# Kernel optimization log

Hardware: AMD Instinct MI355X
Metric: run time of the kernel (lower is better)

## Reference

```python
import jax, jax.numpy as jnp
import numpy as np

N = 20000
E = 320000
H = 16
C = 16
NUM_GRAPHS = 64
NEG_SLOPE = 0.2


def _gat(x, edge_index, W, a_src, a_dst, bias):
    # PyG GATConv, concat=True, shared lin for src/dst, eval mode (no dropout)
    h = (x @ W).reshape(-1, H, C)                       # [N,H,C]
    src, dst = edge_index[0], edge_index[1]
    alpha_src = jnp.sum(h * a_src, axis=-1)             # [N,H]
    alpha_dst = jnp.sum(h * a_dst, axis=-1)             # [N,H]
    alpha = alpha_src[src] + alpha_dst[dst]             # [E,H]
    alpha = jax.nn.leaky_relu(alpha, NEG_SLOPE)
    amax = jax.ops.segment_max(alpha, dst, num_segments=N)
    ex = jnp.exp(alpha - amax[dst])
    denom = jax.ops.segment_sum(ex, dst, num_segments=N)
    attn = ex / jnp.where(denom == 0, 1.0, denom)[dst]  # [E,H]
    msg = h[src] * attn[:, :, None]                     # [E,H,C]
    out = jax.ops.segment_sum(msg, dst, num_segments=N) # [N,H,C]
    return out.reshape(-1, H * C) + bias


def setup_inputs() -> dict:
    key = jax.random.key(0)
    ks = jax.random.split(key, 32)
    d = {}
    d['x'] = jax.random.normal(ks[0], (N, 20), dtype=jnp.float32)
    d['edge_index_ipv6'] = jax.random.randint(ks[1], (2, E), 0, N)
    d['edge_attr_ipv6'] = jax.random.normal(ks[2], (E, 19), dtype=jnp.float32)
    d['edge_index_tsch'] = jax.random.randint(ks[3], (2, E), 0, N)
    d['edge_attr_tsch'] = jax.random.normal(ks[4], (E, 7), dtype=jnp.float32)
    d['batch'] = jnp.sort(jax.random.randint(ks[5], (N,), 0, NUM_GRAPHS))
    s = 0.1
    d['W_i'] = jax.random.normal(ks[6], (20, H * C), dtype=jnp.float32) * s
    d['a_src_i'] = jax.random.normal(ks[7], (H, C), dtype=jnp.float32) * s
    d['a_dst_i'] = jax.random.normal(ks[8], (H, C), dtype=jnp.float32) * s
    d['b_i'] = jnp.zeros((H * C,), dtype=jnp.float32)
    d['W_t'] = jax.random.normal(ks[9], (20, H * C), dtype=jnp.float32) * s
    d['a_src_t'] = jax.random.normal(ks[10], (H, C), dtype=jnp.float32) * s
    d['a_dst_t'] = jax.random.normal(ks[11], (H, C), dtype=jnp.float32) * s
    d['b_t'] = jnp.zeros((H * C,), dtype=jnp.float32)
    d['Wf'] = jax.random.normal(ks[12], (512, 64), dtype=jnp.float32) * s
    d['bf'] = jnp.zeros((64,), dtype=jnp.float32)
    d['W1'] = jax.random.normal(ks[13], (64, 32), dtype=jnp.float32) * s
    d['b1'] = jnp.zeros((32,), dtype=jnp.float32)
    d['W2'] = jax.random.normal(ks[14], (32, 16), dtype=jnp.float32) * s
    d['b2'] = jnp.zeros((16,), dtype=jnp.float32)
    d['W3'] = jax.random.normal(ks[15], (16, 16), dtype=jnp.float32) * s
    d['b3'] = jnp.zeros((16,), dtype=jnp.float32)
    d['Wce'] = jax.random.normal(ks[16], (16, 3), dtype=jnp.float32) * s
    d['bce'] = jnp.zeros((3,), dtype=jnp.float32)
    d['Wcv'] = jax.random.normal(ks[17], (16, 3), dtype=jnp.float32) * s
    d['bcv'] = jnp.zeros((3,), dtype=jnp.float32)
    return d


def reference(x, edge_index_ipv6, edge_attr_ipv6, edge_index_tsch, edge_attr_tsch,
              batch, W_i, a_src_i, a_dst_i, b_i, W_t, a_src_t, a_dst_t, b_t,
              Wf, bf, W1, b1, W2, b2, W3, b3, Wce, bce, Wcv, bcv):
    # edge_attr_* are ignored by GATConv (edge_dim=None in PyG), as in original
    n_ipv6 = _gat(x, edge_index_ipv6, W_i, a_src_i, a_dst_i, b_i)
    n_tsch = _gat(x, edge_index_tsch, W_t, a_src_t, a_dst_t, b_t)
    h = jnp.concatenate([n_ipv6, n_tsch], axis=-1)      # [N,512]
    h = jax.nn.relu(h @ Wf + bf)
    h = jax.nn.relu(h @ W1 + b1)
    h = jax.nn.relu(h @ W2 + b2)
    h = jax.nn.relu(h @ W3 + b3)                        # [N,16]
    ssum = jax.ops.segment_sum(h, batch, num_segments=NUM_GRAPHS)
    cnt = jax.ops.segment_sum(jnp.ones((h.shape[0], 1), h.dtype), batch,
                              num_segments=NUM_GRAPHS)
    g = ssum / jnp.where(cnt == 0, 1.0, cnt)            # [G,16]
    out_event = g @ Wce + bce
    out_env = g @ Wcv + bcv
    return out_event, out_env
```

## Files before the change

kernel.cpp:

```cpp
#include <hip/hip_runtime.h>
#include <math.h>

#define N_NODES 20000
#define N_EDGES 320000
#define NG 64
#define NEG 0.2f
#define NCHUNK ((N_NODES + 255) / 256)

typedef __attribute__((ext_vector_type(8))) short bf16x8;
typedef __attribute__((ext_vector_type(4))) float f32x4;

__device__ __forceinline__ unsigned short f2bf(float f) {
  unsigned int u = __float_as_uint(f);
  return (unsigned short)((u + 0x7fffu + ((u >> 16) & 1u)) >> 16);
}

__global__ __launch_bounds__(256) void k_prep(
    const float* __restrict__ W_i, const float* __restrict__ as_i, const float* __restrict__ ad_i,
    const float* __restrict__ W_t, const float* __restrict__ as_t, const float* __restrict__ ad_t,
    const float* __restrict__ Wf, const float* __restrict__ bf,
    const float* __restrict__ b_i, const float* __restrict__ b_t,
    float* __restrict__ wsall, unsigned short* __restrict__ wbigfrag,
    float* __restrict__ bfold,
    int* __restrict__ fill_i, int* __restrict__ fill_t,
    float* __restrict__ gsum, int* __restrict__ gcnt) {
  __shared__ float bred[4][64];
  int idx = blockIdx.x * 256 + threadIdx.x;
  if (idx < 1280) {
    int k = idx >> 6, c = idx & 63;
    int set = c >> 5, role = (c >> 4) & 1, h = c & 15;
    const float* W = set ? W_t : W_i;
    const float* a = set ? (role ? ad_t : as_t) : (role ? ad_i : as_i);
    float v = 0.f;
#pragma unroll
    for (int j = 0; j < 16; ++j) v = fmaf(W[k * 256 + h * 16 + j], a[h * 16 + j], v);
    wsall[idx] = v;
    return;
  }
  idx -= 1280;
  if (idx < 49152) {
    int ct = idx / 12288, rem = idx % 12288;
    int lane = (rem >> 3) & 63, j = rem & 7, ks = rem >> 9;
    int k = ks * 32 + ((lane >> 4) << 3) + j;
    int nc = ct * 16 + (lane & 15);
    float v = 0.f;
    int g = (k >= 384) ? 1 : 0;
    int r = k - g * 384;
    int h = r / 24, c = r - h * 24;
    if (c < 20) {
      const float* W = g ? W_t : W_i;
      const float* wr = W + c * 256 + (h << 4);
      const float* wf = Wf + ((g << 8) + (h << 4)) * 64 + nc;
#pragma unroll
      for (int m = 0; m < 16; ++m) v = fmaf(wr[m], wf[m * 64], v);
    }
    wbigfrag[idx] = f2bf(v);
    return;
  }
  idx -= 49152;
  if (idx < 256) {
    int t = threadIdx.x, wv = t >> 6, j = t & 63;
    float p = 0.f;
    int i0 = wv * 128;
#pragma unroll 4
    for (int i = i0; i < i0 + 128; ++i) {
      float b = (i < 256) ? b_i[i] : b_t[i - 256];
      p = fmaf(b, Wf[i * 64 + j], p);
    }
    bred[wv][j] = p;
    __syncthreads();
    if (wv == 0) bfold[j] = bred[0][j] + bred[1][j] + bred[2][j] + bred[3][j] + bf[j];
    return;
  }
  idx -= 256;
  if (idx < N_NODES) { fill_i[idx] = 0; return; }
  idx -= N_NODES;
  if (idx < N_NODES) { fill_t[idx] = 0; return; }
  idx -= N_NODES;
  if (idx < NG * 16) { gsum[idx] = 0.f; return; }
  idx -= NG * 16;
  if (idx < NG) gcnt[idx] = 0;
}

__global__ __launch_bounds__(256) void k_alpha(
    const float* __restrict__ x, const float* __restrict__ wsall,
    float* __restrict__ xpad,
    float* __restrict__ asrc0, float* __restrict__ adst0,
    float* __restrict__ asrc1, float* __restrict__ adst1) {
  int t = threadIdx.x;
  int n0 = blockIdx.x * 16;
  __shared__ float xs[16][20];
  __shared__ float ws[20][64];
  for (int i = t; i < 16 * 20; i += 256) {
    int nd = i / 20, k = i % 20;
    xs[nd][k] = x[(n0 + nd) * 20 + k];
  }
  for (int i = t; i < 1280; i += 256) ws[i >> 6][i & 63] = wsall[i];
  __syncthreads();
  for (int i = t; i < 512; i += 256) {
    int nd = i >> 5, j = i & 31;
    xpad[(size_t)(n0 + nd) * 32 + j] = (j < 20) ? xs[nd][j] : 0.f;
  }
#pragma unroll
  for (int i = 0; i < 4; ++i) {
    int wi = i * 256 + t;
    int nd = wi >> 6, c = wi & 63;
    float v = 0.f;
#pragma unroll
    for (int k = 0; k < 20; ++k) v = fmaf(xs[nd][k], ws[k][c], v);
    int n = n0 + nd, h = c & 15;
    float* arr = (c >> 5) ? ((c >> 4) & 1 ? adst1 : asrc1)
                          : ((c >> 4) & 1 ? adst0 : asrc0);
    arr[n * 16 + h] = v;
  }
}

__global__ void k_hist(const int* __restrict__ ei0, const int* __restrict__ ei1,
                       int* __restrict__ cnt0, int* __restrict__ cnt1) {
  int e = blockIdx.x * blockDim.x + threadIdx.x;
  if (e >= N_EDGES) return;
  if (blockIdx.y == 0)
    atomicAdd(&cnt0[ei0[N_EDGES + e]], 1);
  else
    atomicAdd(&cnt1[ei1[N_EDGES + e]], 1);
}

__global__ __launch_bounds__(256) void k_scan1(
    const int* __restrict__ cnt0, const int* __restrict__ cnt1,
    int* __restrict__ tmp0, int* __restrict__ tmp1, int* __restrict__ csums) {
  int chunk = blockIdx.x, set = blockIdx.y;
  const int* cnt = set ? cnt1 : cnt0;
  int* tmp = set ? tmp1 : tmp0;
  int t = threadIdx.x, lane = t & 63, wv = t >> 6;
  int i = chunk * 256 + t;
  int v = (i < N_NODES) ? cnt[i] : 0;
  int s = v;
#pragma unroll
  for (int d = 1; d < 64; d <<= 1) {
    int o = __shfl_up(s, d);
    if (lane >= d) s += o;
  }
  __shared__ int wsum[4];
  if (lane == 63) wsum[wv] = s;
  __syncthreads();
  int pre = 0;
#pragma unroll
  for (int j = 0; j < 4; ++j)
    if (j < wv) pre += wsum[j];
  s += pre;
  if (i < N_NODES) tmp[i] = s;
  if (t == 255) csums[set * 128 + chunk] = s;
}

__global__ __launch_bounds__(256) void k_scan3(
    const int* __restrict__ tmp0, const int* __restrict__ tmp1,
    const int* __restrict__ csums,
    int* __restrict__ rp0, int* __restrict__ rp1,
    int* __restrict__ fill0, int* __restrict__ fill1) {
  int chunk = blockIdx.x, set = blockIdx.y;
  const int* tmp = set ? tmp1 : tmp0;
  int* rp = set ? rp1 : rp0;
  int* fill = set ? fill1 : fill0;
  __shared__ int soff;
  if (threadIdx.x == 0) {
    int acc = 0;
    for (int cc = 0; cc < chunk; ++cc) acc += csums[set * 128 + cc];
    soff = acc;
  }
  __syncthreads();
  int off = soff;
  int i = chunk * 256 + threadIdx.x;
  if (i >= N_NODES) return;
  int incl = tmp[i];
  int c = fill[i];
  int excl = off + incl - c;
  rp[i] = excl;
  fill[i] = excl;
  if (i == N_NODES - 1) rp[N_NODES] = off + incl;
}

__global__ void k_scatter(const int* __restrict__ ei0, const int* __restrict__ ei1,
                          int* __restrict__ fill0, int* __restrict__ fill1,
                          unsigned short* __restrict__ srcs0,
                          unsigned short* __restrict__ srcs1) {
  int e = blockIdx.x * blockDim.x + threadIdx.x;
  if (e >= N_EDGES) return;
  const int* ei = blockIdx.y ? ei1 : ei0;
  int* fill = blockIdx.y ? fill1 : fill0;
  unsigned short* srcs = blockIdx.y ? srcs1 : srcs0;
  int d = ei[N_EDGES + e];
  int pos = atomicAdd(&fill[d], 1);
  srcs[pos] = (unsigned short)ei[e];
}

__global__ __launch_bounds__(256) void k_gat(
    const float* __restrict__ xpad,
    const float* __restrict__ asrc0, const float* __restrict__ adst0,
    const float* __restrict__ asrc1, const float* __restrict__ adst1,
    const int* __restrict__ rp0, const unsigned short* __restrict__ srcs0,
    const int* __restrict__ rp1, const unsigned short* __restrict__ srcs1,
    unsigned short* __restrict__ xagg) {
  __shared__ float lds[4][416];
  int w4 = threadIdx.x >> 6, lane = threadIdx.x & 63;
  int n = blockIdx.x * 2 + (w4 >> 1);
  int g = w4 & 1;
  int h16 = lane & 15, e4 = lane >> 4;
  float* lxs = lds[w4];
  float* lat = lds[w4] + 288;

  const float* asrc = g ? asrc1 : asrc0;
  const float* adst = g ? adst1 : adst0;
  const int* rp = g ? rp1 : rp0;
  const unsigned short* srcs = g ? srcs1 : srcs0;
  int k0 = rp[n], k1 = rp[n + 1];
  int deg = k1 - k0;
  float adn = adst[n * 16 + h16];
  float lacc = 0.f;
  float xa[8];
#pragma unroll
  for (int j = 0; j < 8; ++j) xa[j] = 0.f;

  if (deg > 0) {
    int nbat = (deg + 7) >> 3;
    int s0a = (int)srcs[min(k0 + e4, k1 - 1)];
    int s0b = (int)srcs[min(k0 + 4 + e4, k1 - 1)];
    float av0a = asrc[s0a * 16 + h16];
    float av0b = asrc[s0b * 16 + h16];
    float2 xv0a = *(const float2*)&xpad[(size_t)s0a * 32 + h16 * 2];
    float2 xv0b = *(const float2*)&xpad[(size_t)s0b * 32 + h16 * 2];
    int s1a = 0, s1b = 0;
    if (nbat > 1) {
      s1a = (int)srcs[min(k0 + 8 + e4, k1 - 1)];
      s1b = (int)srcs[min(k0 + 12 + e4, k1 - 1)];
    }
    for (int bb = 0; bb < nbat; ++bb) {
      float av1a = 0.f, av1b = 0.f;
      float2 xv1a = {0.f, 0.f}, xv1b = {0.f, 0.f};
      int s2a = 0, s2b = 0;
      if (bb + 1 < nbat) {
        av1a = asrc[s1a * 16 + h16];
        av1b = asrc[s1b * 16 + h16];
        xv1a = *(const float2*)&xpad[(size_t)s1a * 32 + h16 * 2];
        xv1b = *(const float2*)&xpad[(size_t)s1b * 32 + h16 * 2];
      }
      if (bb + 2 < nbat) {
        int kb = k0 + (bb + 2) * 8;
        s2a = (int)srcs[min(kb + e4, k1 - 1)];
        s2b = (int)srcs[min(kb + 4 + e4, k1 - 1)];
      }
      int base = k0 + bb * 8;
      float a1 = av0a + adn; a1 = a1 >= 0.f ? a1 : NEG * a1;
      float a2 = av0b + adn; a2 = a2 >= 0.f ? a2 : NEG * a2;
      float exa = (base + e4 < k1) ? __expf(a1) : 0.f;
      float exb = (base + 4 + e4 < k1) ? __expf(a2) : 0.f;
      lacc += exa + exb;
      lat[e4 * 16 + h16] = exa;
      lat[(4 + e4) * 16 + h16] = exb;
      *(float2*)&lxs[e4 * 36 + h16 * 2] = xv0a;
      *(float2*)&lxs[(4 + e4) * 36 + h16 * 2] = xv0b;
#pragma unroll
      for (int e = 0; e < 8; ++e) {
        float w = lat[e * 16 + h16];
        const float4 x0 = *(const float4*)&lxs[e * 36 + e4 * 8];
        const float4 x1 = *(const float4*)&lxs[e * 36 + e4 * 8 + 4];
        xa[0] = fmaf(w, x0.x, xa[0]); xa[1] = fmaf(w, x0.y, xa[1]);
        xa[2] = fmaf(w, x0.z, xa[2]); xa[3] = fmaf(w, x0.w, xa[3]);
        xa[4] = fmaf(w, x1.x, xa[4]); xa[5] = fmaf(w, x1.y, xa[5]);
        xa[6] = fmaf(w, x1.z, xa[6]); xa[7] = fmaf(w, x1.w, xa[7]);
      }
      av0a = av1a; av0b = av1b; xv0a = xv1a; xv0b = xv1b;
      s0a = s1a; s0b = s1b; s1a = s2a; s1b = s2b;
    }
  }
  float lh = lacc + __shfl_xor(lacc, 16);
  lh += __shfl_xor(lh, 32);
  float invl = lh > 0.f ? 1.f / lh : 0.f;
  if (e4 < 3) {
    unsigned int u[4];
#pragma unroll
    for (int q = 0; q < 4; ++q)
      u[q] = (unsigned int)f2bf(xa[2 * q] * invl) |
             ((unsigned int)f2bf(xa[2 * q + 1] * invl) << 16);
    *(uint4*)&xagg[(size_t)n * 768 + g * 384 + h16 * 24 + e4 * 8] = *(uint4*)u;
  }
}

__global__ __launch_bounds__(256) void k_mlp(
    const unsigned short* __restrict__ xagg, const unsigned short* __restrict__ wbigfrag,
    const float* __restrict__ bfold,
    const float* __restrict__ W1m, const float* __restrict__ b1v,
    const float* __restrict__ W2m, const float* __restrict__ b2v,
    const float* __restrict__ W3m, const float* __restrict__ b3v,
    const int* __restrict__ batch,
    float* __restrict__ gsum, int* __restrict__ gcnt) {
  int t = threadIdx.x, w = t >> 6, lane = t & 63;
  int n0 = blockIdx.x * 64;
  __shared__ float o1[64][68];
  __shared__ float o2[64][36];
  __shared__ float o3[64][20];
  __shared__ float o4[64][17];
  __shared__ int bs[64];
  if (t < 64) bs[t] = batch[min(n0 + t, N_NODES - 1)];

  {
    int m = lane & 15, kb = lane >> 4;
    int arow = n0 + w * 16 + m;
    if (arow >= N_NODES) arow = N_NODES - 1;
    const unsigned short* aptr = xagg + (size_t)arow * 768 + kb * 8;
    f32x4 acc0 = {0.f, 0.f, 0.f, 0.f}, acc1 = acc0, acc2 = acc0, acc3 = acc0;
#pragma unroll 4
    for (int ks = 0; ks < 24; ++ks) {
      bf16x8 af = *(const bf16x8*)(aptr + ks * 32);
      const unsigned short* bks = wbigfrag + (size_t)ks * 512 + lane * 8;
      bf16x8 b0 = *(const bf16x8*)(bks);
      bf16x8 b1 = *(const bf16x8*)(bks + 12288);
      bf16x8 b2 = *(const bf16x8*)(bks + 24576);
      bf16x8 b3 = *(const bf16x8*)(bks + 36864);
      acc0 = __builtin_amdgcn_mfma_f32_16x16x32_bf16(af, b0, acc0, 0, 0, 0);
      acc1 = __builtin_amdgcn_mfma_f32_16x16x32_bf16(af, b1, acc1, 0, 0, 0);
      acc2 = __builtin_amdgcn_mfma_f32_16x16x32_bf16(af, b2, acc2, 0, 0, 0);
      acc3 = __builtin_amdgcn_mfma_f32_16x16x32_bf16(af, b3, acc3, 0, 0, 0);
    }
    int col = lane & 15, rg = lane >> 4;
#pragma unroll
    for (int r = 0; r < 4; ++r) {
      int row = w * 16 + rg * 4 + r;
      o1[row][col]      = fmaxf(acc0[r] + bfold[col], 0.f);
      o1[row][16 + col] = fmaxf(acc1[r] + bfold[16 + col], 0.f);
      o1[row][32 + col] = fmaxf(acc2[r] + bfold[32 + col], 0.f);
      o1[row][48 + col] = fmaxf(acc3[r] + bfold[48 + col], 0.f);
    }
  }
  __syncthreads();
  int nd = t >> 2, qo = t & 3;
  {
    float a[8];
#pragma unroll
    for (int j = 0; j < 8; ++j) a[j] = b1v[qo * 8 + j];
#pragma unroll 4
    for (int k = 0; k < 64; ++k) {
      float hv = o1[nd][k];
      const float4 wA = *(const float4*)&W1m[k * 32 + qo * 8];
      const float4 wB = *(const float4*)&W1m[k * 32 + qo * 8 + 4];
      a[0] = fmaf(hv, wA.x, a[0]); a[1] = fmaf(hv, wA.y, a[1]);
      a[2] = fmaf(hv, wA.z, a[2]); a[3] = fmaf(hv, wA.w, a[3]);
      a[4] = fmaf(hv, wB.x, a[4]); a[5] = fmaf(hv, wB.y, a[5]);
      a[6] = fmaf(hv, wB.z, a[6]); a[7] = fmaf(hv, wB.w, a[7]);
    }
#pragma unroll
    for (int j = 0; j < 8; ++j) o2[nd][qo * 8 + j] = fmaxf(a[j], 0.f);
  }
  __syncthreads();
  {
    float a[4];
    const float4 bb = *(const float4*)&b2v[qo * 4];
    a[0] = bb.x; a[1] = bb.y; a[2] = bb.z; a[3] = bb.w;
#pragma unroll 4
    for (int k = 0; k < 32; ++k) {
      float hv = o2[nd][k];
      const float4 ww = *(const float4*)&W2m[k * 16 + qo * 4];
      a[0] = fmaf(hv, ww.x, a[0]); a[1] = fmaf(hv, ww.y, a[1]);
      a[2] = fmaf(hv, ww.z, a[2]); a[3] = fmaf(hv, ww.w, a[3]);
    }
#pragma unroll
    for (int j = 0; j < 4; ++j) o3[nd][qo * 4 + j] = fmaxf(a[j], 0.f);
  }
  __syncthreads();
  {
    float a[4];
    const float4 bb = *(const float4*)&b3v[qo * 4];
    a[0] = bb.x; a[1] = bb.y; a[2] = bb.z; a[3] = bb.w;
#pragma unroll
    for (int k = 0; k < 16; ++k) {
      float hv = o3[nd][k];
      const float4 ww = *(const float4*)&W3m[k * 16 + qo * 4];
      a[0] = fmaf(hv, ww.x, a[0]); a[1] = fmaf(hv, ww.y, a[1]);
      a[2] = fmaf(hv, ww.z, a[2]); a[3] = fmaf(hv, ww.w, a[3]);
    }
#pragma unroll
    for (int j = 0; j < 4; ++j) o4[nd][qo * 4 + j] = fmaxf(a[j], 0.f);
  }
  __syncthreads();
  if (t < 128) {
    int s = t >> 4, js = t & 15;
    int b = bs[0] + s;
    if (b <= bs[63]) {
      float sum = 0.f; int c = 0;
#pragma unroll 8
      for (int ndd = 0; ndd < 64; ++ndd) {
        if (n0 + ndd < N_NODES && bs[ndd] == b) { sum += o4[ndd][js]; ++c; }
      }
      if (c > 0) {
        atomicAdd(&gsum[b * 16 + js], sum);
        if (js == 0) atomicAdd(&gcnt[b], c);
      }
    }
  }
}

__global__ void k_head(const float* __restrict__ gsum, const int* __restrict__ gcnt,
                       const float* __restrict__ Wce, const float* __restrict__ bce,
                       const float* __restrict__ Wcv, const float* __restrict__ bcv,
                       float* __restrict__ out) {
  int t = threadIdx.x;
  if (t >= 384) return;
  int half = t / 192, idx = t % 192;
  int b = idx / 3, r = idx % 3;
  float cnt = (float)gcnt[b];
  float inv = cnt > 0.f ? 1.f / cnt : 1.f;
  const float* Wc = half ? Wcv : Wce;
  const float* bc = half ? bcv : bce;
  float v = bc[r];
#pragma unroll
  for (int j = 0; j < 16; ++j) v = fmaf(gsum[b * 16 + j] * inv, Wc[j * 3 + r], v);
  out[t] = v;
}

extern "C" void kernel_launch(void* const* d_in, const int* in_sizes, int n_in,
                              void* d_out, int out_size, void* d_ws, size_t ws_size,
                              hipStream_t stream) {
  const float* x = (const float*)d_in[0];
  const int* ei_i = (const int*)d_in[1];
  const int* ei_t = (const int*)d_in[3];
  const int* batch = (const int*)d_in[5];
  const float* W_i = (const float*)d_in[6];
  const float* as_i = (const float*)d_in[7];
  const float* ad_i = (const float*)d_in[8];
  const float* b_i = (const float*)d_in[9];
  const float* W_t = (const float*)d_in[10];
  const float* as_t = (const float*)d_in[11];
  const float* ad_t = (const float*)d_in[12];
  const float* b_t = (const float*)d_in[13];
  const float* Wf = (const float*)d_in[14];
  const float* bf = (const float*)d_in[15];
  const float* W1 = (const float*)d_in[16];
  const float* b1 = (const float*)d_in[17];
  const float* W2 = (const float*)d_in[18];
  const float* b2 = (const float*)d_in[19];
  const float* W3 = (const float*)d_in[20];
  const float* b3 = (const float*)d_in[21];
  const float* Wce = (const float*)d_in[22];
  const float* bce = (const float*)d_in[23];
  const float* Wcv = (const float*)d_in[24];
  const float* bcv = (const float*)d_in[25];

  char* ws = (char*)d_ws;
  size_t off = 0;
  auto take = [&](size_t bytes) {
    void* p = ws + off;
    off = (off + bytes + 255) & ~(size_t)255;
    return p;
  };
  float* xpad = (float*)take((size_t)N_NODES * 32 * 4);
  unsigned short* xagg = (unsigned short*)take((size_t)N_NODES * 768 * 2);
  float* wsall = (float*)take((size_t)1280 * 4);
  unsigned short* wbigfrag = (unsigned short*)take((size_t)49152 * 2);
  float* bfold = (float*)take((size_t)64 * 4);
  float* asrc_i = (float*)take((size_t)N_NODES * 16 * 4);
  float* adst_i = (float*)take((size_t)N_NODES * 16 * 4);
  float* asrc_t = (float*)take((size_t)N_NODES * 16 * 4);
  float* adst_t = (float*)take((size_t)N_NODES * 16 * 4);
  int* rowptr_i = (int*)take((size_t)(N_NODES + 1) * 4);
  int* rowptr_t = (int*)take((size_t)(N_NODES + 1) * 4);
  int* fill_i = (int*)take((size_t)N_NODES * 4);
  int* fill_t = (int*)take((size_t)N_NODES * 4);
  int* tmp_i = (int*)take((size_t)N_NODES * 4);
  int* tmp_t = (int*)take((size_t)N_NODES * 4);
  int* csums = (int*)take((size_t)2 * 128 * 4);
  unsigned short* srcs_i = (unsigned short*)take((size_t)N_EDGES * 2);
  unsigned short* srcs_t = (unsigned short*)take((size_t)N_EDGES * 2);
  float* gsum = (float*)take((size_t)NG * 16 * 4);
  int* gcnt = (int*)take((size_t)NG * 4);

  int prep_items = 1280 + 49152 + 256 + N_NODES + N_NODES + NG * 16 + NG;
  k_prep<<<(prep_items + 255) / 256, 256, 0, stream>>>(
      W_i, as_i, ad_i, W_t, as_t, ad_t, Wf, bf, b_i, b_t,
      wsall, wbigfrag, bfold, fill_i, fill_t, gsum, gcnt);

  k_alpha<<<N_NODES / 16, 256, 0, stream>>>(x, wsall, xpad,
                                            asrc_i, adst_i, asrc_t, adst_t);

  dim3 egrid((N_EDGES + 255) / 256, 2);
  k_hist<<<egrid, 256, 0, stream>>>(ei_i, ei_t, fill_i, fill_t);
  dim3 sgrid(NCHUNK, 2);
  k_scan1<<<sgrid, 256, 0, stream>>>(fill_i, fill_t, tmp_i, tmp_t, csums);
  k_scan3<<<sgrid, 256, 0, stream>>>(tmp_i, tmp_t, csums, rowptr_i, rowptr_t,
                                     fill_i, fill_t);
  k_scatter<<<egrid, 256, 0, stream>>>(ei_i, ei_t, fill_i, fill_t, srcs_i, srcs_t);

  k_gat<<<N_NODES / 2, 256, 0, stream>>>(xpad, asrc_i, adst_i, asrc_t, adst_t,
                                         rowptr_i, srcs_i, rowptr_t, srcs_t,
                                         xagg);

  k_mlp<<<(N_NODES + 63) / 64, 256, 0, stream>>>(xagg, wbigfrag, bfold,
                                                 W1, b1, W2, b2, W3, b3,
                                                 batch, gsum, gcnt);

  k_head<<<1, 384, 0, stream>>>(gsum, gcnt, Wce, bce, Wcv, bcv, (float*)d_out);
}
```

Before: 158.2 us.

## Batch 16 edges per GAT iteration and split MLP across waves by output columns

The GAT aggregation kernel now processes 16 edges per loop iteration. Source indices are loaded once per lane and broadcast with shuffles, and each lane loads a float4 pair of source features instead of float2s. This replaces the two-stage software prefetch pipeline with a single-step index prefetch, aiming to cut per-edge loop overhead and issue fewer, wider loads. The MLP kernel now uses 16-node blocks with each wave computing one 16-column MFMA tile, which gives four times as many blocks for occupancy but reloads A fragments per wave and issues more atomics.

```diff
diff --git a/kernel.cpp b/kernel.cpp
--- a/kernel.cpp
+++ b/kernel.cpp
@@ -200,76 +200,56 @@
     const int* __restrict__ rp0, const unsigned short* __restrict__ srcs0,
     const int* __restrict__ rp1, const unsigned short* __restrict__ srcs1,
     unsigned short* __restrict__ xagg) {
-  __shared__ float lds[4][416];
+  __shared__ float xsh[4][16][36];
+  __shared__ float lath[4][16][16];
   int w4 = threadIdx.x >> 6, lane = threadIdx.x & 63;
   int n = blockIdx.x * 2 + (w4 >> 1);
   int g = w4 & 1;
   int h16 = lane & 15, e4 = lane >> 4;
-  float* lxs = lds[w4];
-  float* lat = lds[w4] + 288;
-
+  int eid = lane & 15, slot = lane >> 4;
+  float (*xs)[36] = xsh[w4];
+  float (*la)[16] = lath[w4];
   const float* asrc = g ? asrc1 : asrc0;
   const float* adst = g ? adst1 : adst0;
   const int* rp = g ? rp1 : rp0;
   const unsigned short* srcs = g ? srcs1 : srcs0;
   int k0 = rp[n], k1 = rp[n + 1];
-  int deg = k1 - k0;
   float adn = adst[n * 16 + h16];
   float lacc = 0.f;
   float xa[8];
 #pragma unroll
   for (int j = 0; j < 8; ++j) xa[j] = 0.f;
-
-  if (deg > 0) {
-    int nbat = (deg + 7) >> 3;
-    int s0a = (int)srcs[min(k0 + e4, k1 - 1)];
-    int s0b = (int)srcs[min(k0 + 4 + e4, k1 - 1)];
-    float av0a = asrc[s0a * 16 + h16];
-    float av0b = asrc[s0b * 16 + h16];
-    float2 xv0a = *(const float2*)&xpad[(size_t)s0a * 32 + h16 * 2];
-    float2 xv0b = *(const float2*)&xpad[(size_t)s0b * 32 + h16 * 2];
-    int s1a = 0, s1b = 0;
-    if (nbat > 1) {
-      s1a = (int)srcs[min(k0 + 8 + e4, k1 - 1)];
-      s1b = (int)srcs[min(k0 + 12 + e4, k1 - 1)];
-    }
-    for (int bb = 0; bb < nbat; ++bb) {
-      float av1a = 0.f, av1b = 0.f;
-      float2 xv1a = {0.f, 0.f}, xv1b = {0.f, 0.f};
-      int s2a = 0, s2b = 0;
-      if (bb + 1 < nbat) {
-        av1a = asrc[s1a * 16 + h16];
-        av1b = asrc[s1b * 16 + h16];
-        xv1a = *(const float2*)&xpad[(size_t)s1a * 32 + h16 * 2];
-        xv1b = *(const float2*)&xpad[(size_t)s1b * 32 + h16 * 2];
+  if (k1 > k0) {
+    int sb = (int)srcs[min(k0 + eid, k1 - 1)];
+    for (int base = k0; base < k1; base += 16) {
+      int sbN = 0;
+      if (base + 16 < k1) sbN = (int)srcs[min(base + 16 + eid, k1 - 1)];
+      float4 xv0 = *(const float4*)&xpad[(size_t)sb * 32 + slot * 8];
+      float4 xv1 = *(const float4*)&xpad[(size_t)sb * 32 + slot * 8 + 4];
+      float ex[4];
+#pragma unroll
+      for (int q = 0; q < 4; ++q) {
+        int e = e4 + 4 * q;
+        int s = __shfl(sb, e);
+        float aa = asrc[s * 16 + h16] + adn;
+        aa = aa >= 0.f ? aa : NEG * aa;
+        ex[q] = (base + e < k1) ? __expf(aa) : 0.f;
+        lacc += ex[q];
+        la[e][h16] = ex[q];
       }
-      if (bb + 2 < nbat) {
-        int kb = k0 + (bb + 2) * 8;
-        s2a = (int)srcs[min(kb + e4, k1 - 1)];
-        s2b = (int)srcs[min(kb + 4 + e4, k1 - 1)];
-      }
-      int base = k0 + bb * 8;
-      float a1 = av0a + adn; a1 = a1 >= 0.f ? a1 : NEG * a1;
-      float a2 = av0b + adn; a2 = a2 >= 0.f ? a2 : NEG * a2;
-      float exa = (base + e4 < k1) ? __expf(a1) : 0.f;
-      float exb = (base + 4 + e4 < k1) ? __expf(a2) : 0.f;
-      lacc += exa + exb;
-      lat[e4 * 16 + h16] = exa;
-      lat[(4 + e4) * 16 + h16] = exb;
-      *(float2*)&lxs[e4 * 36 + h16 * 2] = xv0a;
-      *(float2*)&lxs[(4 + e4) * 36 + h16 * 2] = xv0b;
-#pragma unroll
-      for (int e = 0; e < 8; ++e) {
-        float w = lat[e * 16 + h16];
-        const float4 x0 = *(const float4*)&lxs[e * 36 + e4 * 8];
-        const float4 x1 = *(const float4*)&lxs[e * 36 + e4 * 8 + 4];
+      *(float4*)&xs[eid][slot * 8] = xv0;
+      *(float4*)&xs[eid][slot * 8 + 4] = xv1;
+#pragma unroll
+      for (int e = 0; e < 16; ++e) {
+        float w = la[e][h16];
+        float4 x0 = *(const float4*)&xs[e][e4 * 8];
+        float4 x1 = *(const float4*)&xs[e][e4 * 8 + 4];
         xa[0] = fmaf(w, x0.x, xa[0]); xa[1] = fmaf(w, x0.y, xa[1]);
         xa[2] = fmaf(w, x0.z, xa[2]); xa[3] = fmaf(w, x0.w, xa[3]);
         xa[4] = fmaf(w, x1.x, xa[4]); xa[5] = fmaf(w, x1.y, xa[5]);
         xa[6] = fmaf(w, x1.z, xa[6]); xa[7] = fmaf(w, x1.w, xa[7]);
       }
-      av0a = av1a; av0b = av1b; xv0a = xv1a; xv0b = xv1b;
-      s0a = s1a; s0b = s1b; s1a = s2a; s1b = s2b;
+      sb = sbN;
     }
   }
   float lh = lacc + __shfl_xor(lacc, 16);
@@ -294,105 +274,71 @@
     const int* __restrict__ batch,
     float* __restrict__ gsum, int* __restrict__ gcnt) {
   int t = threadIdx.x, w = t >> 6, lane = t & 63;
-  int n0 = blockIdx.x * 64;
-  __shared__ float o1[64][68];
-  __shared__ float o2[64][36];
-  __shared__ float o3[64][20];
-  __shared__ float o4[64][17];
-  __shared__ int bs[64];
-  if (t < 64) bs[t] = batch[min(n0 + t, N_NODES - 1)];
+  int n0 = blockIdx.x * 16;
+  __shared__ float o1[16][68];
+  __shared__ float o2[16][36];
+  __shared__ float o3[16][20];
+  __shared__ float o4[16][17];
+  __shared__ int bs[16];
+  if (t < 16) bs[t] = batch[n0 + t];
 
   {
     int m = lane & 15, kb = lane >> 4;
-    int arow = n0 + w * 16 + m;
-    if (arow >= N_NODES) arow = N_NODES - 1;
-    const unsigned short* aptr = xagg + (size_t)arow * 768 + kb * 8;
-    f32x4 acc0 = {0.f, 0.f, 0.f, 0.f}, acc1 = acc0, acc2 = acc0, acc3 = acc0;
-#pragma unroll 4
+    const unsigned short* aptr = xagg + (size_t)(n0 + m) * 768 + kb * 8;
+    const unsigned short* bbase = wbigfrag + (size_t)w * 12288 + lane * 8;
+    f32x4 acc = {0.f, 0.f, 0.f, 0.f};
+#pragma unroll 6
     for (int ks = 0; ks < 24; ++ks) {
       bf16x8 af = *(const bf16x8*)(aptr + ks * 32);
-      const unsigned short* bks = wbigfrag + (size_t)ks * 512 + lane * 8;
-      bf16x8 b0 = *(const bf16x8*)(bks);
-      bf16x8 b1 = *(const bf16x8*)(bks + 12288);
-      bf16x8 b2 = *(const bf16x8*)(bks + 24576);
-      bf16x8 b3 = *(const bf16x8*)(bks + 36864);
-      acc0 = __builtin_amdgcn_mfma_f32_16x16x32_bf16(af, b0, acc0, 0, 0, 0);
-      acc1 = __builtin_amdgcn_mfma_f32_16x16x32_bf16(af, b1, acc1, 0, 0, 0);
-      acc2 = __builtin_amdgcn_mfma_f32_16x16x32_bf16(af, b2, acc2, 0, 0, 0);
-      acc3 = __builtin_amdgcn_mfma_f32_16x16x32_bf16(af, b3, acc3, 0, 0, 0);
+      bf16x8 bfr = *(const bf16x8*)(bbase + (size_t)ks * 512);
+      acc = __builtin_amdgcn_mfma_f32_16x16x32_bf16(af, bfr, acc, 0, 0, 0);
     }
     int col = lane & 15, rg = lane >> 4;
 #pragma unroll
     for (int r = 0; r < 4; ++r) {
-      int row = w * 16 + rg * 4 + r;
-      o1[row][col]      = fmaxf(acc0[r] + bfold[col], 0.f);
-      o1[row][16 + col] = fmaxf(acc1[r] + bfold[16 + col], 0.f);
-      o1[row][32 + col] = fmaxf(acc2[r] + bfold[32 + col], 0.f);
-      o1[row][48 + col] = fmaxf(acc3[r] + bfold[48 + col], 0.f);
-    }
-  }
-  __syncthreads();
-  int nd = t >> 2, qo = t & 3;
+      int row = rg * 4 + r;
+      o1[row][w * 16 + col] = fmaxf(acc[r] + bfold[w * 16 + col], 0.f);
+    }
+  }
+  __syncthreads();
+  int nd = t >> 4, js = t & 15;
   {
-    float a[8];
-#pragma unroll
-    for (int j = 0; j < 8; ++j) a[j] = b1v[qo * 8 + j];
-#pragma unroll 4
+    float a0 = b1v[js], a1 = b1v[js + 16];
+#pragma unroll 8
     for (int k = 0; k < 64; ++k) {
       float hv = o1[nd][k];
-      const float4 wA = *(const float4*)&W1m[k * 32 + qo * 8];
-      const float4 wB = *(const float4*)&W1m[k * 32 + qo * 8 + 4];
-      a[0] = fmaf(hv, wA.x, a[0]); a[1] = fmaf(hv, wA.y, a[1]);
-      a[2] = fmaf(hv, wA.z, a[2]); a[3] = fmaf(hv, wA.w, a[3]);
-      a[4] = fmaf(hv, wB.x, a[4]); a[5] = fmaf(hv, wB.y, a[5]);
-      a[6] = fmaf(hv, wB.z, a[6]); a[7] = fmaf(hv, wB.w, a[7]);
-    }
-#pragma unroll
-    for (int j = 0; j < 8; ++j) o2[nd][qo * 8 + j] = fmaxf(a[j], 0.f);
+      a0 = fmaf(hv, W1m[k * 32 + js], a0);
+      a1 = fmaf(hv, W1m[k * 32 + js + 16], a1);
+    }
+    o2[nd][js] = fmaxf(a0, 0.f);
+    o2[nd][js + 16] = fmaxf(a1, 0.f);
   }
   __syncthreads();
   {
-    float a[4];
-    const float4 bb = *(const float4*)&b2v[qo * 4];
-    a[0] = bb.x; a[1] = bb.y; a[2] = bb.z; a[3] = bb.w;
-#pragma unroll 4
-    for (int k = 0; k < 32; ++k) {
-      float hv = o2[nd][k];
-      const float4 ww = *(const float4*)&W2m[k * 16 + qo * 4];
-      a[0] = fmaf(hv, ww.x, a[0]); a[1] = fmaf(hv, ww.y, a[1]);
-      a[2] = fmaf(hv, ww.z, a[2]); a[3] = fmaf(hv, ww.w, a[3]);
-    }
-#pragma unroll
-    for (int j = 0; j < 4; ++j) o3[nd][qo * 4 + j] = fmaxf(a[j], 0.f);
+    float a = b2v[js];
+#pragma unroll
+    for (int k = 0; k < 32; ++k) a = fmaf(o2[nd][k], W2m[k * 16 + js], a);
+    o3[nd][js] = fmaxf(a, 0.f);
   }
   __syncthreads();
   {
-    float a[4];
-    const float4 bb = *(const float4*)&b3v[qo * 4];
-    a[0] = bb.x; a[1] = bb.y; a[2] = bb.z; a[3] = bb.w;
-#pragma unroll
-    for (int k = 0; k < 16; ++k) {
-      float hv = o3[nd][k];
-      const float4 ww = *(const float4*)&W3m[k * 16 + qo * 4];
-      a[0] = fmaf(hv, ww.x, a[0]); a[1] = fmaf(hv, ww.y, a[1]);
-      a[2] = fmaf(hv, ww.z, a[2]); a[3] = fmaf(hv, ww.w, a[3]);
-    }
-#pragma unroll
-    for (int j = 0; j < 4; ++j) o4[nd][qo * 4 + j] = fmaxf(a[j], 0.f);
+    float a = b3v[js];
+#pragma unroll
+    for (int k = 0; k < 16; ++k) a = fmaf(o3[nd][k], W3m[k * 16 + js], a);
+    o4[nd][js] = fmaxf(a, 0.f);
   }
   __syncthreads();
   if (t < 128) {
-    int s = t >> 4, js = t & 15;
+    int s = t >> 4, jx = t & 15;
     int b = bs[0] + s;
-    if (b <= bs[63]) {
+    if (b <= bs[15]) {
       float sum = 0.f; int c = 0;
-#pragma unroll 8
-      for (int ndd = 0; ndd < 64; ++ndd) {
-        if (n0 + ndd < N_NODES && bs[ndd] == b) { sum += o4[ndd][js]; ++c; }
-      }
+#pragma unroll
+      for (int ndd = 0; ndd < 16; ++ndd)
+        if (bs[ndd] == b) { sum += o4[ndd][jx]; ++c; }
       if (c > 0) {
-        atomicAdd(&gsum[b * 16 + js], sum);
-        if (js == 0) atomicAdd(&gcnt[b], c);
+        atomicAdd(&gsum[b * 16 + jx], sum);
+        if (jx == 0) atomicAdd(&gcnt[b], c);
       }
     }
   }
@@ -492,9 +438,9 @@
                                          rowptr_i, srcs_i, rowptr_t, srcs_t,
                                          xagg);
 
-  k_mlp<<<(N_NODES + 63) / 64, 256, 0, stream>>>(xagg, wbigfrag, bfold,
-                                                 W1, b1, W2, b2, W3, b3,
-                                                 batch, gsum, gcnt);
+  k_mlp<<<N_NODES / 16, 256, 0, stream>>>(xagg, wbigfrag, bfold,
+                                          W1, b1, W2, b2, W3, b3,
+                                          batch, gsum, gcnt);
 
   k_head<<<1, 384, 0, stream>>>(gsum, gcnt, Wce, bce, Wcv, bcv, (float*)d_out);
 }
```

Result: slower. 163.1 us (+3.1%).
